# Kernel optimization log

Measured on AMD Instinct MI355X. Metric: run time of the kernel, lower is better.

## Reference

```python
import jax, jax.numpy as jnp
import numpy as np

NUM_INST = 3
N_NODES = 50000
IN_F = 128
HID = 64
HEADS = 4
HF = HEADS * HID  # 256
NEG_SLOPE = 0.2
BN_EPS = 1e-5


def setup_inputs() -> dict:
    key = jax.random.key(0)
    ks = jax.random.split(key, 10)
    sppmi = jax.random.normal(ks[0], (NUM_INST, N_NODES, IN_F), dtype=jnp.float32)
    edge_index = jax.random.randint(ks[1], (2, 800000), 0, N_NODES, dtype=jnp.int64)
    # Per-instance GATConv params (lin_src weight, att_src/att_dst, bias), BN, and Linear
    s = 1.0 / np.sqrt(IN_F)
    W = jax.random.uniform(ks[2], (NUM_INST, HF, IN_F), jnp.float32, -s, s)
    att_src = jax.random.uniform(ks[3], (NUM_INST, HEADS, HID), jnp.float32, -s, s)
    att_dst = jax.random.uniform(ks[4], (NUM_INST, HEADS, HID), jnp.float32, -s, s)
    bias = jnp.zeros((NUM_INST, HF), jnp.float32)
    bn_gamma = jnp.ones((NUM_INST, HF), jnp.float32)
    bn_beta = jnp.zeros((NUM_INST, HF), jnp.float32)
    bn_mean = jnp.zeros((NUM_INST, HF), jnp.float32)
    bn_var = jnp.ones((NUM_INST, HF), jnp.float32)
    s2 = 1.0 / np.sqrt(HF)
    lin_W = jax.random.uniform(ks[5], (NUM_INST, HID, HF), jnp.float32, -s2, s2)
    lin_b = jax.random.uniform(ks[6], (NUM_INST, HID), jnp.float32, -s2, s2)
    return {"sppmi": sppmi, "W": W, "att_src": att_src, "att_dst": att_dst,
            "bias": bias, "bn_gamma": bn_gamma, "bn_beta": bn_beta,
            "bn_mean": bn_mean, "bn_var": bn_var, "lin_W": lin_W,
            "lin_b": lin_b, "edge_index": edge_index}


def _gat_layer(x, W, a_src, a_dst, bias, gamma, beta, mean, var, linW, linb, src, dst):
    # GATConv (concat=True, add_self_loops already applied via src/dst)
    xw = (x @ W.T).reshape(N_NODES, HEADS, HID)            # [N,H,F]
    alpha_src = (xw * a_src).sum(-1)                        # [N,H]
    alpha_dst = (xw * a_dst).sum(-1)                        # [N,H]
    e = jax.nn.leaky_relu(alpha_src[src] + alpha_dst[dst], NEG_SLOPE)  # [E,H]
    m = jax.ops.segment_max(e, dst, num_segments=N_NODES)  # segment softmax over dst
    e = jnp.exp(e - m[dst])
    denom = jax.ops.segment_sum(e, dst, num_segments=N_NODES)
    alpha = e / (denom[dst] + 1e-16)                        # [E,H]
    msg = alpha[:, :, None] * xw[src]                       # [E,H,F] gather-attend
    out = jax.ops.segment_sum(msg, dst, num_segments=N_NODES)  # scatter-add
    out = out.reshape(N_NODES, HF) + bias
    # BatchNorm1d (eval: running stats), ReLU, Linear
    out = (out - mean) * jax.lax.rsqrt(var + BN_EPS) * gamma + beta
    out = jax.nn.relu(out)
    return out @ linW.T + linb                              # [N,HID]


def reference(sppmi, W, att_src, att_dst, bias, bn_gamma, bn_beta, bn_mean, bn_var, lin_W, lin_b, edge_index):
    loop = jnp.arange(N_NODES, dtype=edge_index.dtype)
    src = jnp.concatenate([edge_index[0], loop])
    dst = jnp.concatenate([edge_index[1], loop])
    all_emb = jnp.zeros((N_NODES, HID), jnp.float32)
    for i in range(NUM_INST):
        all_emb = all_emb + _gat_layer(sppmi[i], W[i], att_src[i], att_dst[i], bias[i],
                                       bn_gamma[i], bn_beta[i], bn_mean[i], bn_var[i],
                                       lin_W[i], lin_b[i], src, dst)
    out_1 = all_emb / jnp.linalg.norm(all_emb, axis=1, keepdims=True)
    return out_1
```

## Files before the change

kernel.cpp:

```cpp
#include <hip/hip_runtime.h>
#include <hip/hip_bf16.h>

#define N_NODES 50000
#define E0      800000
#define ET      850000
#define IN_F    128
#define HF      256
#define HID     64
#define NEG     0.2f
#define BN_EPSC 1e-5f
#define NSCAN_BLK 196

typedef __attribute__((ext_vector_type(8))) short bh8;
typedef __attribute__((ext_vector_type(4))) float fl4;
typedef __attribute__((ext_vector_type(8))) unsigned short us8;

__device__ __forceinline__ float lrelu(float x){ return x > 0.f ? x : NEG * x; }
__device__ __forceinline__ unsigned short f2b(float f){
  unsigned int x = __float_as_uint(f);
  unsigned int r = x + 0x7FFF + ((x >> 16) & 1);
  return (unsigned short)(r >> 16);
}
__device__ __forceinline__ float b2f(unsigned short u){
  return __uint_as_float((unsigned int)u << 16);
}

#define NW4 (3 * HF * IN_F / 4)
#define NL4 (3 * HID * HF / 4)
__global__ __launch_bounds__(256) void k_prep(const float* __restrict__ W, unsigned short* __restrict__ wb,
                                              const float* __restrict__ linW, unsigned short* __restrict__ lwb,
                                              const float* __restrict__ g, const float* __restrict__ b,
                                              const float* __restrict__ m, const float* __restrict__ v,
                                              float* __restrict__ scale, float* __restrict__ shiftv){
  int idx = blockIdx.x * 256 + threadIdx.x;
  if (idx < NW4){
    float4 x = ((const float4*)W)[idx];
    ((ushort4*)wb)[idx] = make_ushort4(f2b(x.x), f2b(x.y), f2b(x.z), f2b(x.w));
  } else if (idx < NW4 + NL4){
    int j = idx - NW4;
    float4 x = ((const float4*)linW)[j];
    ((ushort4*)lwb)[j] = make_ushort4(f2b(x.x), f2b(x.y), f2b(x.z), f2b(x.w));
  } else if (idx < NW4 + NL4 + 3 * HF){
    int i = idx - NW4 - NL4;
    float s = g[i] * rsqrtf(v[i] + BN_EPSC);
    scale[i] = s;
    shiftv[i] = b[i] - m[i] * s;
  }
}

__global__ void k_hist(const int* __restrict__ ei, int* __restrict__ counts){
  int e = blockIdx.x * 256 + threadIdx.x;
  if (e >= ET) return;
  int d = (e < E0) ? ei[E0 + e] : (e - E0);
  atomicAdd(&counts[d], 1);
}

__global__ __launch_bounds__(256) void k_bsum(const int* __restrict__ counts, int* __restrict__ bsums){
  int b = blockIdx.x;
  int t = threadIdx.x;
  int idx = b * 256 + t;
  int v = (idx < N_NODES) ? counts[idx] : 0;
  for (int m = 1; m < 64; m <<= 1) v += __shfl_xor(v, m, 64);
  __shared__ int ws[4];
  int lane = t & 63, w = t >> 6;
  if (lane == 0) ws[w] = v;
  __syncthreads();
  if (t == 0) bsums[b] = ws[0] + ws[1] + ws[2] + ws[3];
}

__global__ __launch_bounds__(256) void k_bscan(const int* __restrict__ bsums, int* __restrict__ bexcl,
                                               int* __restrict__ row_ptr){
  int t = threadIdx.x;
  int v = (t < NSCAN_BLK) ? bsums[t] : 0;
  int lane = t & 63, w = t >> 6;
  int incl = v;
  for (int m = 1; m < 64; m <<= 1){
    int n = __shfl_up(incl, m, 64);
    if (lane >= m) incl += n;
  }
  __shared__ int ws[4];
  if (lane == 63) ws[w] = incl;
  __syncthreads();
  if (t == 0){
    int r = 0;
    for (int j = 0; j < 4; ++j){ int x = ws[j]; ws[j] = r; r += x; }
  }
  __syncthreads();
  int excl = incl - v + ws[w];
  if (t < NSCAN_BLK) bexcl[t] = excl;
  if (t == 255) row_ptr[N_NODES] = excl + v;
}

__global__ __launch_bounds__(256) void k_sfinal(const int* __restrict__ counts,
                                                const int* __restrict__ bexcl,
                                                int* __restrict__ row_ptr, int* __restrict__ cursor){
  int b = blockIdx.x;
  int t = threadIdx.x;
  int idx = b * 256 + t;
  int v = (idx < N_NODES) ? counts[idx] : 0;
  int lane = t & 63, w = t >> 6;
  int incl = v;
  for (int m = 1; m < 64; m <<= 1){
    int n = __shfl_up(incl, m, 64);
    if (lane >= m) incl += n;
  }
  __shared__ int ws[4];
  if (lane == 63) ws[w] = incl;
  __syncthreads();
  if (t == 0){
    int r = 0;
    for (int j = 0; j < 4; ++j){ int x = ws[j]; ws[j] = r; r += x; }
  }
  __syncthreads();
  int excl = incl - v + ws[w];
  int pos = bexcl[b] + excl;
  if (idx < N_NODES){ row_ptr[idx] = pos; cursor[idx] = pos; }
}

__global__ void k_scatter(const int* __restrict__ ei, int* __restrict__ cursor,
                          int* __restrict__ csr_src){
  int e = blockIdx.x * 256 + threadIdx.x;
  if (e >= ET) return;
  int s, d;
  if (e < E0){ s = ei[e]; d = ei[E0 + e]; } else { s = e - E0; d = s; }
  int pos = atomicAdd(&cursor[d], 1);
  csr_src[pos] = s;
}

__global__ __launch_bounds__(256) void k_gemm1f(const float* __restrict__ sppmi,
                                                const unsigned short* __restrict__ wb,
                                                const float* __restrict__ att_src,
                                                const float* __restrict__ att_dst,
                                                unsigned short* __restrict__ xwb,
                                                float* __restrict__ as3, float* __restrict__ ad3){
  __shared__ unsigned char Asm[32 * 256];
  __shared__ unsigned char Bsm[256 * 256];
  int tid = threadIdx.x;
  int bx = blockIdx.x;
  int inst = bx / 1563;
  int m0 = (bx % 1563) * 32;
  const float* x = sppmi + (size_t)inst * N_NODES * IN_F;
  const unsigned short* wbv = wb + (size_t)inst * HF * IN_F;
  const float* asrc = att_src + inst * HF;
  const float* adst = att_dst + inst * HF;
  float* as_ = as3 + (size_t)inst * N_NODES * 4;
  float* ad_ = ad3 + (size_t)inst * N_NODES * 4;
  unsigned short* xw = xwb + (size_t)inst * N_NODES * HF;

  #pragma unroll
  for (int k = 0; k < 4; ++k){
    int c = k * 256 + tid;
    int row = c >> 5;
    int c4 = c & 31;
    int grow = m0 + row; if (grow >= N_NODES) grow = N_NODES - 1;
    float4 v = *(const float4*)&x[(size_t)grow * IN_F + c4 * 4];
    ushort4 o = make_ushort4(f2b(v.x), f2b(v.y), f2b(v.z), f2b(v.w));
    int colb = c4 * 8;
    int addr = row * 256 + ((colb & ~15) ^ ((row & 7) << 4)) + (colb & 15);
    *(ushort4*)(Asm + addr) = o;
  }
  #pragma unroll
  for (int k = 0; k < 16; ++k){
    int c = k * 256 + tid;
    int row = c >> 4;
    int colb = (c & 15) * 16;
    uint4 v = *(const uint4*)((const char*)wbv + (size_t)row * 256 + colb);
    *(uint4*)(Bsm + row * 256 + (colb ^ ((row & 7) << 4))) = v;
  }
  __syncthreads();

  int w = tid >> 6, lane = tid & 63;
  int l15 = lane & 15, l4 = lane >> 4;
  fl4 acc[2][4] = {};
  #pragma unroll
  for (int kk = 0; kk < 4; ++kk){
    bh8 af[2];
    #pragma unroll
    for (int m = 0; m < 2; ++m){
      int ar = m * 16 + l15;
      int ac = (kk * 64 + l4 * 16) ^ ((ar & 7) << 4);
      af[m] = *(const bh8*)(Asm + ar * 256 + ac);
    }
    bh8 bfv[4];
    #pragma unroll
    for (int n = 0; n < 4; ++n){
      int br = w * 64 + n * 16 + l15;
      int bc = (kk * 64 + l4 * 16) ^ ((br & 7) << 4);
      bfv[n] = *(const bh8*)(Bsm + br * 256 + bc);
    }
    #pragma unroll
    for (int m = 0; m < 2; ++m)
      #pragma unroll
      for (int n = 0; n < 4; ++n)
        acc[m][n] = __builtin_amdgcn_mfma_f32_16x16x32_bf16(af[m], bfv[n], acc[m][n], 0, 0, 0);
  }

  float asv[4], adv[4];
  #pragma unroll
  for (int n = 0; n < 4; ++n){
    int c = w * 64 + n * 16 + l15;
    asv[n] = asrc[c]; adv[n] = adst[c];
  }

  #pragma unroll
  for (int m = 0; m < 2; ++m){
    #pragma unroll
    for (int j = 0; j < 4; ++j){
      int grow = m0 + m * 16 + l4 * 4 + j;
      if (grow < N_NODES){
        #pragma unroll
        for (int n = 0; n < 4; ++n)
          xw[(size_t)grow * HF + w * 64 + n * 16 + l15] = f2b(acc[m][n][j]);
      }
      float ts = acc[m][0][j]*asv[0] + acc[m][1][j]*asv[1] + acc[m][2][j]*asv[2] + acc[m][3][j]*asv[3];
      float td = acc[m][0][j]*adv[0] + acc[m][1][j]*adv[1] + acc[m][2][j]*adv[2] + acc[m][3][j]*adv[3];
      #pragma unroll
      for (int mm = 1; mm < 16; mm <<= 1){ ts += __shfl_xor(ts, mm, 64); td += __shfl_xor(td, mm, 64); }
      if (l15 == 0 && grow < N_NODES){
        as_[grow * 4 + w] = ts;
        ad_[grow * 4 + w] = td;
      }
    }
  }
}

__global__ __launch_bounds__(256) void k_agg3(const unsigned short* __restrict__ xwb,
                     const float* __restrict__ as3, const float* __restrict__ ad3,
                     const int* __restrict__ row_ptr, const int* __restrict__ csr_src,
                     const float* __restrict__ bias, unsigned short* __restrict__ outb){
  __shared__ float eLds[4][4][65];
  __shared__ int   sLds[4][64];
  int bx = blockIdx.x;
  int inst = bx / 12500;
  int chunk = bx - inst * 12500;
  int w = threadIdx.x >> 6;
  int lane = threadIdx.x & 63;
  int node = chunk * 4 + w;
  int row0 = row_ptr[node];
  int deg = row_ptr[node + 1] - row0;
  const float* as_ = as3 + (size_t)inst * N_NODES * 4;
  const float* ad_ = ad3 + (size_t)inst * N_NODES * 4;
  float4 ad4 = *(const float4*)&ad_[node * 4];
  int h = lane >> 4;
  float accx = 0.f, accy = 0.f, accz = 0.f, accw = 0.f;
  float sh;
  const char* xwp = (const char*)(xwb + (size_t)inst * N_NODES * HF);
  int lb = lane * 8;

  if (deg <= 64){
    int soff = 0; float e0 = 0.f, e1 = 0.f, e2 = 0.f, e3 = 0.f;
    if (lane < deg){
      int sreg = csr_src[row0 + lane];
      soff = sreg * 512;
      float4 a4 = *(const float4*)&as_[sreg * 4];
      e0 = __expf(lrelu(a4.x + ad4.x));
      e1 = __expf(lrelu(a4.y + ad4.y));
      e2 = __expf(lrelu(a4.z + ad4.z));
      e3 = __expf(lrelu(a4.w + ad4.w));
    }
    sLds[w][lane] = soff;
    eLds[w][0][lane] = e0; eLds[w][1][lane] = e1;
    eLds[w][2][lane] = e2; eLds[w][3][lane] = e3;
    float s0 = e0, s1 = e1, s2 = e2, s3 = e3;
    for (int m = 1; m < 64; m <<= 1){
      s0 += __shfl_xor(s0, m, 64); s1 += __shfl_xor(s1, m, 64);
      s2 += __shfl_xor(s2, m, 64); s3 += __shfl_xor(s3, m, 64);
    }
    sh = (h == 0) ? s0 : (h == 1) ? s1 : (h == 2) ? s2 : s3;
    int q = 0;
    for (; q + 4 <= deg; q += 4){
      int o0 = sLds[w][q],   o1 = sLds[w][q+1];
      int o2 = sLds[w][q+2], o3 = sLds[w][q+3];
      float w0 = eLds[w][h][q],   w1 = eLds[w][h][q+1];
      float w2 = eLds[w][h][q+2], w3 = eLds[w][h][q+3];
      ushort4 u0 = *(const ushort4*)(xwp + o0 + lb);
      ushort4 u1 = *(const ushort4*)(xwp + o1 + lb);
      ushort4 u2 = *(const ushort4*)(xwp + o2 + lb);
      ushort4 u3 = *(const ushort4*)(xwp + o3 + lb);
      accx += w0*b2f(u0.x) + w1*b2f(u1.x) + w2*b2f(u2.x) + w3*b2f(u3.x);
      accy += w0*b2f(u0.y) + w1*b2f(u1.y) + w2*b2f(u2.y) + w3*b2f(u3.y);
      accz += w0*b2f(u0.z) + w1*b2f(u1.z) + w2*b2f(u2.z) + w3*b2f(u3.z);
      accw += w0*b2f(u0.w) + w1*b2f(u1.w) + w2*b2f(u2.w) + w3*b2f(u3.w);
    }
    for (; q < deg; ++q){
      int o0 = sLds[w][q];
      float wh = eLds[w][h][q];
      ushort4 u = *(const ushort4*)(xwp + o0 + lb);
      accx += wh * b2f(u.x); accy += wh * b2f(u.y);
      accz += wh * b2f(u.z); accw += wh * b2f(u.w);
    }
  } else {
    float s0 = 0.f, s1 = 0.f, s2 = 0.f, s3 = 0.f;
    for (int j = lane; j < deg; j += 64){
      int s = csr_src[row0 + j];
      float4 a4 = *(const float4*)&as_[s * 4];
      s0 += __expf(lrelu(a4.x + ad4.x));
      s1 += __expf(lrelu(a4.y + ad4.y));
      s2 += __expf(lrelu(a4.z + ad4.z));
      s3 += __expf(lrelu(a4.w + ad4.w));
    }
    for (int m = 1; m < 64; m <<= 1){
      s0 += __shfl_xor(s0, m, 64); s1 += __shfl_xor(s1, m, 64);
      s2 += __shfl_xor(s2, m, 64); s3 += __shfl_xor(s3, m, 64);
    }
    sh = (h == 0) ? s0 : (h == 1) ? s1 : (h == 2) ? s2 : s3;
    for (int jb = 0; jb < deg; jb += 64){
      int jj = jb + lane;
      int soff = 0; float e0 = 0.f, e1 = 0.f, e2 = 0.f, e3 = 0.f;
      if (jj < deg){
        int sreg = csr_src[row0 + jj];
        soff = sreg * 512;
        float4 a4 = *(const float4*)&as_[sreg * 4];
        e0 = __expf(lrelu(a4.x + ad4.x));
        e1 = __expf(lrelu(a4.y + ad4.y));
        e2 = __expf(lrelu(a4.z + ad4.z));
        e3 = __expf(lrelu(a4.w + ad4.w));
      }
      sLds[w][lane] = soff;
      eLds[w][0][lane] = e0; eLds[w][1][lane] = e1;
      eLds[w][2][lane] = e2; eLds[w][3][lane] = e3;
      __builtin_amdgcn_s_waitcnt(0);
      int lim = min(64, deg - jb);
      for (int q = 0; q < lim; ++q){
        int o0 = sLds[w][q];
        float wh = eLds[w][h][q];
        ushort4 u = *(const ushort4*)(xwp + o0 + lb);
        accx += wh * b2f(u.x); accy += wh * b2f(u.y);
        accz += wh * b2f(u.z); accw += wh * b2f(u.w);
      }
    }
  }
  float invh = 1.f / (sh + 1e-16f);
  const float* bi = bias + inst * HF;
  float4 b4 = *(const float4*)&bi[lane * 4];
  ushort4 o;
  o.x = f2b(accx * invh + b4.x); o.y = f2b(accy * invh + b4.y);
  o.z = f2b(accz * invh + b4.z); o.w = f2b(accw * invh + b4.w);
  *(ushort4*)&outb[(size_t)inst * N_NODES * HF + (size_t)node * HF + lane * 4] = o;
}

__global__ __launch_bounds__(256) void k_gemm2f(const unsigned short* __restrict__ obase,
                                                const unsigned short* __restrict__ lwb,
                                                const float* __restrict__ scale,
                                                const float* __restrict__ shiftv,
                                                const float* __restrict__ linb,
                                                float* __restrict__ outp){
  __shared__ unsigned char Asm[64 * 512];
  __shared__ unsigned char Bsm[64 * 512];
  int tid = threadIdx.x;
  int m0 = blockIdx.x * 64;
  int w = tid >> 6, lane = tid & 63;
  int l15 = lane & 15, l4 = lane >> 4;

  fl4 acc[4] = {};

  for (int i = 0; i < 3; ++i){
    if (i) __syncthreads();
    const unsigned short* A = obase + (size_t)i * N_NODES * HF;
    const float* sc = scale + i * HF;
    const float* sf = shiftv + i * HF;
    #pragma unroll
    for (int k = 0; k < 8; ++k){
      int c = k * 256 + tid;
      int row = c >> 5;
      int colb = (c & 31) * 16;
      int col = colb >> 1;
      int grow = m0 + row; if (grow >= N_NODES) grow = N_NODES - 1;
      us8 u = *(const us8*)&A[(size_t)grow * HF + col];
      float4 s0 = *(const float4*)&sc[col], s1 = *(const float4*)&sc[col + 4];
      float4 f0 = *(const float4*)&sf[col], f1 = *(const float4*)&sf[col + 4];
      us8 o;
      o[0] = f2b(fmaxf(0.f, b2f(u[0]) * s0.x + f0.x));
      o[1] = f2b(fmaxf(0.f, b2f(u[1]) * s0.y + f0.y));
      o[2] = f2b(fmaxf(0.f, b2f(u[2]) * s0.z + f0.z));
      o[3] = f2b(fmaxf(0.f, b2f(u[3]) * s0.w + f0.w));
      o[4] = f2b(fmaxf(0.f, b2f(u[4]) * s1.x + f1.x));
      o[5] = f2b(fmaxf(0.f, b2f(u[5]) * s1.y + f1.y));
      o[6] = f2b(fmaxf(0.f, b2f(u[6]) * s1.z + f1.z));
      o[7] = f2b(fmaxf(0.f, b2f(u[7]) * s1.w + f1.w));
      *(us8*)(Asm + row * 512 + (colb ^ ((row & 7) << 4))) = o;
    }
    const unsigned short* B = lwb + (size_t)i * HID * HF;
    #pragma unroll
    for (int k = 0; k < 8; ++k){
      int c = k * 256 + tid;
      int row = c >> 5;
      int colb = (c & 31) * 16;
      uint4 v = *(const uint4*)((const char*)B + (size_t)row * 512 + colb);
      *(uint4*)(Bsm + row * 512 + (colb ^ ((row & 7) << 4))) = v;
    }
    __syncthreads();
    #pragma unroll
    for (int kk = 0; kk < 8; ++kk){
      int ar = w * 16 + l15;
      int ac = (kk * 64 + l4 * 16) ^ ((ar & 7) << 4);
      bh8 af = *(const bh8*)(Asm + ar * 512 + ac);
      #pragma unroll
      for (int n = 0; n < 4; ++n){
        int br = n * 16 + l15;
        int bc = (kk * 64 + l4 * 16) ^ ((br & 7) << 4);
        bh8 bfv = *(const bh8*)(Bsm + br * 512 + bc);
        acc[n] = __builtin_amdgcn_mfma_f32_16x16x32_bf16(af, bfv, acc[n], 0, 0, 0);
      }
    }
  }
  float lbs[4];
  #pragma unroll
  for (int n = 0; n < 4; ++n){
    int c = n * 16 + l15;
    lbs[n] = linb[c] + linb[64 + c] + linb[128 + c];
  }
  #pragma unroll
  for (int j = 0; j < 4; ++j){
    float v0 = acc[0][j] + lbs[0];
    float v1 = acc[1][j] + lbs[1];
    float v2 = acc[2][j] + lbs[2];
    float v3 = acc[3][j] + lbs[3];
    float ss = v0*v0 + v1*v1 + v2*v2 + v3*v3;
    #pragma unroll
    for (int mm = 1; mm < 16; mm <<= 1) ss += __shfl_xor(ss, mm, 64);
    float rn = 1.f / sqrtf(ss);
    int grow = m0 + w * 16 + l4 * 4 + j;
    if (grow < N_NODES){
      float* op = outp + (size_t)grow * HID;
      op[l15]      = v0 * rn;
      op[16 + l15] = v1 * rn;
      op[32 + l15] = v2 * rn;
      op[48 + l15] = v3 * rn;
    }
  }
}

extern "C" void kernel_launch(void* const* d_in, const int* in_sizes, int n_in,
                              void* d_out, int out_size, void* d_ws, size_t ws_size,
                              hipStream_t stream){
  const float* sppmi   = (const float*)d_in[0];
  const float* W       = (const float*)d_in[1];
  const float* att_src = (const float*)d_in[2];
  const float* att_dst = (const float*)d_in[3];
  const float* bias    = (const float*)d_in[4];
  const float* bn_g    = (const float*)d_in[5];
  const float* bn_b    = (const float*)d_in[6];
  const float* bn_m    = (const float*)d_in[7];
  const float* bn_v    = (const float*)d_in[8];
  const float* lin_W   = (const float*)d_in[9];
  const float* lin_b   = (const float*)d_in[10];
  const int*   ei      = (const int*)d_in[11];

  char* ws = (char*)d_ws;
  size_t off = 0;
  auto alloc = [&](size_t bytes)->char*{ char* p = ws + off; off += (bytes + 255) & ~(size_t)255; return p; };
  unsigned short* wb   = (unsigned short*)alloc((size_t)3 * HF * IN_F * 2);
  unsigned short* lwb  = (unsigned short*)alloc((size_t)3 * HID * HF * 2);
  float* scale  = (float*)alloc((size_t)3 * HF * 4);
  float* shiftv = (float*)alloc((size_t)3 * HF * 4);
  unsigned short* xwb  = (unsigned short*)alloc((size_t)3 * N_NODES * HF * 2);
  unsigned short* outb = (unsigned short*)alloc((size_t)3 * N_NODES * HF * 2);
  float* as3    = (float*)alloc((size_t)3 * N_NODES * 4 * 4);
  float* ad3    = (float*)alloc((size_t)3 * N_NODES * 4 * 4);
  int* counts   = (int*)alloc((size_t)N_NODES * 4);
  int* row_ptr  = (int*)alloc((size_t)(N_NODES + 4) * 4);
  int* cursor   = (int*)alloc((size_t)N_NODES * 4);
  int* csr      = (int*)alloc((size_t)ET * 4);
  int* bsums    = (int*)alloc((size_t)NSCAN_BLK * 4);
  int* bexcl    = (int*)alloc((size_t)NSCAN_BLK * 4);

  hipMemsetAsync(counts, 0, (size_t)N_NODES * 4, stream);

  k_prep<<<147, 256, 0, stream>>>(W, wb, lin_W, lwb, bn_g, bn_b, bn_m, bn_v, scale, shiftv);

  k_hist<<<(ET + 255) / 256, 256, 0, stream>>>(ei, counts);
  k_bsum<<<NSCAN_BLK, 256, 0, stream>>>(counts, bsums);
  k_bscan<<<1, 256, 0, stream>>>(bsums, bexcl, row_ptr);
  k_sfinal<<<NSCAN_BLK, 256, 0, stream>>>(counts, bexcl, row_ptr, cursor);
  k_scatter<<<(ET + 255) / 256, 256, 0, stream>>>(ei, cursor, csr);

  k_gemm1f<<<3 * 1563, 256, 0, stream>>>(sppmi, wb, att_src, att_dst, xwb, as3, ad3);
  k_agg3<<<37500, 256, 0, stream>>>(xwb, as3, ad3, row_ptr, csr, bias, outb);
  k_gemm2f<<<782, 256, 0, stream>>>(outb, lwb, scale, shiftv, lin_b, (float*)d_out);
}
```

Measured before the change: 361.2 us.

## Permute xw column layout for vector stores, fuse scan kernels, persistent aggregation grid

The first GEMM now writes its bf16 output as packed ushort4 stores in a permuted column order instead of four scattered 2-byte stores. The bias, BN scale/shift and linear weights are pre-permuted in the prep kernel to match that order. The single-block block-scan kernel is merged into the final scan kernel, with every block redundantly scanning the block sums, which removes one launch. The aggregation kernel becomes a grid-stride persistent loop over 2048 blocks instead of 37500, trading launch and scheduling overhead for possible load imbalance.

Measured after the change: 371.1 us. +2.7%, slower.

```diff
diff --git a/kernel.cpp b/kernel.cpp
--- a/kernel.cpp
+++ b/kernel.cpp
@@ -10,6 +10,7 @@
 #define NEG     0.2f
 #define BN_EPSC 1e-5f
 #define NSCAN_BLK 196
+#define NCHUNKS 37500
 
 typedef __attribute__((ext_vector_type(8))) short bh8;
 typedef __attribute__((ext_vector_type(4))) float fl4;
@@ -23,6 +24,11 @@
 }
 __device__ __forceinline__ float b2f(unsigned short u){
   return __uint_as_float((unsigned int)u << 16);
+}
+
+__device__ __forceinline__ int perm_true(int cp){
+  int blk = cp & ~63, r = cp & 63;
+  return blk + (r & 3) * 16 + (r >> 2);
 }
 
 #define NW4 (3 * HF * IN_F / 4)
@@ -31,20 +37,33 @@
                                               const float* __restrict__ linW, unsigned short* __restrict__ lwb,
                                               const float* __restrict__ g, const float* __restrict__ b,
                                               const float* __restrict__ m, const float* __restrict__ v,
-                                              float* __restrict__ scale, float* __restrict__ shiftv){
+                                              const float* __restrict__ bias,
+                                              float* __restrict__ scale, float* __restrict__ shiftv,
+                                              float* __restrict__ bias_p){
   int idx = blockIdx.x * 256 + threadIdx.x;
   if (idx < NW4){
     float4 x = ((const float4*)W)[idx];
     ((ushort4*)wb)[idx] = make_ushort4(f2b(x.x), f2b(x.y), f2b(x.z), f2b(x.w));
   } else if (idx < NW4 + NL4){
     int j = idx - NW4;
-    float4 x = ((const float4*)linW)[j];
-    ((ushort4*)lwb)[j] = make_ushort4(f2b(x.x), f2b(x.y), f2b(x.z), f2b(x.w));
+    int j4 = j * 4;
+    int irow = j4 >> 8;
+    int cp = j4 & 255;
+    int blk = cp & ~63, l15 = (cp & 63) >> 2;
+    const float* src = linW + (size_t)irow * HF + blk + l15;
+    ushort4 o = make_ushort4(f2b(src[0]), f2b(src[16]), f2b(src[32]), f2b(src[48]));
+    ((ushort4*)lwb)[j] = o;
   } else if (idx < NW4 + NL4 + 3 * HF){
     int i = idx - NW4 - NL4;
-    float s = g[i] * rsqrtf(v[i] + BN_EPSC);
+    int inst = i >> 8, cp = i & 255;
+    int c = inst * HF + perm_true(cp);
+    float s = g[c] * rsqrtf(v[c] + BN_EPSC);
     scale[i] = s;
-    shiftv[i] = b[i] - m[i] * s;
+    shiftv[i] = b[c] - m[c] * s;
+  } else if (idx < NW4 + NL4 + 6 * HF){
+    int i = idx - NW4 - NL4 - 3 * HF;
+    int inst = i >> 8, cp = i & 255;
+    bias_p[i] = bias[inst * HF + perm_true(cp)];
   }
 }
 
@@ -68,52 +87,37 @@
   if (t == 0) bsums[b] = ws[0] + ws[1] + ws[2] + ws[3];
 }
 
-__global__ __launch_bounds__(256) void k_bscan(const int* __restrict__ bsums, int* __restrict__ bexcl,
-                                               int* __restrict__ row_ptr){
-  int t = threadIdx.x;
-  int v = (t < NSCAN_BLK) ? bsums[t] : 0;
+__global__ __launch_bounds__(256) void k_sfinal(const int* __restrict__ counts,
+                                                const int* __restrict__ bsums,
+                                                int* __restrict__ row_ptr, int* __restrict__ cursor){
+  __shared__ int bex[256];
+  __shared__ int ws0[4];
+  __shared__ int ws[4];
+  int b = blockIdx.x, t = threadIdx.x;
   int lane = t & 63, w = t >> 6;
+  {
+    int v = (t < NSCAN_BLK) ? bsums[t] : 0;
+    int incl = v;
+    for (int m = 1; m < 64; m <<= 1){ int n = __shfl_up(incl, m, 64); if (lane >= m) incl += n; }
+    if (lane == 63) ws0[w] = incl;
+    __syncthreads();
+    if (t == 0){ int r = 0; for (int j = 0; j < 4; ++j){ int x = ws0[j]; ws0[j] = r; r += x; } }
+    __syncthreads();
+    int excl = incl - v + ws0[w];
+    bex[t] = excl;
+    if (b == 0 && t == 255) row_ptr[N_NODES] = excl + v;
+    __syncthreads();
+  }
+  int idx = b * 256 + t;
+  int v = (idx < N_NODES) ? counts[idx] : 0;
   int incl = v;
-  for (int m = 1; m < 64; m <<= 1){
-    int n = __shfl_up(incl, m, 64);
-    if (lane >= m) incl += n;
-  }
-  __shared__ int ws[4];
+  for (int m = 1; m < 64; m <<= 1){ int n = __shfl_up(incl, m, 64); if (lane >= m) incl += n; }
   if (lane == 63) ws[w] = incl;
   __syncthreads();
-  if (t == 0){
-    int r = 0;
-    for (int j = 0; j < 4; ++j){ int x = ws[j]; ws[j] = r; r += x; }
-  }
+  if (t == 0){ int r = 0; for (int j = 0; j < 4; ++j){ int x = ws[j]; ws[j] = r; r += x; } }
   __syncthreads();
   int excl = incl - v + ws[w];
-  if (t < NSCAN_BLK) bexcl[t] = excl;
-  if (t == 255) row_ptr[N_NODES] = excl + v;
-}
-
-__global__ __launch_bounds__(256) void k_sfinal(const int* __restrict__ counts,
-                                                const int* __restrict__ bexcl,
-                                                int* __restrict__ row_ptr, int* __restrict__ cursor){
-  int b = blockIdx.x;
-  int t = threadIdx.x;
-  int idx = b * 256 + t;
-  int v = (idx < N_NODES) ? counts[idx] : 0;
-  int lane = t & 63, w = t >> 6;
-  int incl = v;
-  for (int m = 1; m < 64; m <<= 1){
-    int n = __shfl_up(incl, m, 64);
-    if (lane >= m) incl += n;
-  }
-  __shared__ int ws[4];
-  if (lane == 63) ws[w] = incl;
-  __syncthreads();
-  if (t == 0){
-    int r = 0;
-    for (int j = 0; j < 4; ++j){ int x = ws[j]; ws[j] = r; r += x; }
-  }
-  __syncthreads();
-  int excl = incl - v + ws[w];
-  int pos = bexcl[b] + excl;
+  int pos = bex[b] + excl;
   if (idx < N_NODES){ row_ptr[idx] = pos; cursor[idx] = pos; }
 }
 
@@ -208,9 +212,9 @@
     for (int j = 0; j < 4; ++j){
       int grow = m0 + m * 16 + l4 * 4 + j;
       if (grow < N_NODES){
-        #pragma unroll
-        for (int n = 0; n < 4; ++n)
-          xw[(size_t)grow * HF + w * 64 + n * 16 + l15] = f2b(acc[m][n][j]);
+        ushort4 o4 = make_ushort4(f2b(acc[m][0][j]), f2b(acc[m][1][j]),
+                                  f2b(acc[m][2][j]), f2b(acc[m][3][j]));
+        *(ushort4*)(xw + (size_t)grow * HF + w * 64 + l15 * 4) = o4;
       }
       float ts = acc[m][0][j]*asv[0] + acc[m][1][j]*asv[1] + acc[m][2][j]*asv[2] + acc[m][3][j]*asv[3];
       float td = acc[m][0][j]*adv[0] + acc[m][1][j]*adv[1] + acc[m][2][j]*adv[2] + acc[m][3][j]*adv[3];
@@ -227,89 +231,32 @@
 __global__ __launch_bounds__(256) void k_agg3(const unsigned short* __restrict__ xwb,
                      const float* __restrict__ as3, const float* __restrict__ ad3,
                      const int* __restrict__ row_ptr, const int* __restrict__ csr_src,
-                     const float* __restrict__ bias, unsigned short* __restrict__ outb){
+                     const float* __restrict__ bias_p, unsigned short* __restrict__ outb){
   __shared__ float eLds[4][4][65];
   __shared__ int   sLds[4][64];
-  int bx = blockIdx.x;
-  int inst = bx / 12500;
-  int chunk = bx - inst * 12500;
   int w = threadIdx.x >> 6;
   int lane = threadIdx.x & 63;
-  int node = chunk * 4 + w;
-  int row0 = row_ptr[node];
-  int deg = row_ptr[node + 1] - row0;
-  const float* as_ = as3 + (size_t)inst * N_NODES * 4;
-  const float* ad_ = ad3 + (size_t)inst * N_NODES * 4;
-  float4 ad4 = *(const float4*)&ad_[node * 4];
   int h = lane >> 4;
-  float accx = 0.f, accy = 0.f, accz = 0.f, accw = 0.f;
-  float sh;
-  const char* xwp = (const char*)(xwb + (size_t)inst * N_NODES * HF);
   int lb = lane * 8;
 
-  if (deg <= 64){
-    int soff = 0; float e0 = 0.f, e1 = 0.f, e2 = 0.f, e3 = 0.f;
-    if (lane < deg){
-      int sreg = csr_src[row0 + lane];
-      soff = sreg * 512;
-      float4 a4 = *(const float4*)&as_[sreg * 4];
-      e0 = __expf(lrelu(a4.x + ad4.x));
-      e1 = __expf(lrelu(a4.y + ad4.y));
-      e2 = __expf(lrelu(a4.z + ad4.z));
-      e3 = __expf(lrelu(a4.w + ad4.w));
-    }
-    sLds[w][lane] = soff;
-    eLds[w][0][lane] = e0; eLds[w][1][lane] = e1;
-    eLds[w][2][lane] = e2; eLds[w][3][lane] = e3;
-    float s0 = e0, s1 = e1, s2 = e2, s3 = e3;
-    for (int m = 1; m < 64; m <<= 1){
-      s0 += __shfl_xor(s0, m, 64); s1 += __shfl_xor(s1, m, 64);
-      s2 += __shfl_xor(s2, m, 64); s3 += __shfl_xor(s3, m, 64);
-    }
-    sh = (h == 0) ? s0 : (h == 1) ? s1 : (h == 2) ? s2 : s3;
-    int q = 0;
-    for (; q + 4 <= deg; q += 4){
-      int o0 = sLds[w][q],   o1 = sLds[w][q+1];
-      int o2 = sLds[w][q+2], o3 = sLds[w][q+3];
-      float w0 = eLds[w][h][q],   w1 = eLds[w][h][q+1];
-      float w2 = eLds[w][h][q+2], w3 = eLds[w][h][q+3];
-      ushort4 u0 = *(const ushort4*)(xwp + o0 + lb);
-      ushort4 u1 = *(const ushort4*)(xwp + o1 + lb);
-      ushort4 u2 = *(const ushort4*)(xwp + o2 + lb);
-      ushort4 u3 = *(const ushort4*)(xwp + o3 + lb);
-      accx += w0*b2f(u0.x) + w1*b2f(u1.x) + w2*b2f(u2.x) + w3*b2f(u3.x);
-      accy += w0*b2f(u0.y) + w1*b2f(u1.y) + w2*b2f(u2.y) + w3*b2f(u3.y);
-      accz += w0*b2f(u0.z) + w1*b2f(u1.z) + w2*b2f(u2.z) + w3*b2f(u3.z);
-      accw += w0*b2f(u0.w) + w1*b2f(u1.w) + w2*b2f(u2.w) + w3*b2f(u3.w);
-    }
-    for (; q < deg; ++q){
-      int o0 = sLds[w][q];
-      float wh = eLds[w][h][q];
-      ushort4 u = *(const ushort4*)(xwp + o0 + lb);
-      accx += wh * b2f(u.x); accy += wh * b2f(u.y);
-      accz += wh * b2f(u.z); accw += wh * b2f(u.w);
-    }
-  } else {
-    float s0 = 0.f, s1 = 0.f, s2 = 0.f, s3 = 0.f;
-    for (int j = lane; j < deg; j += 64){
-      int s = csr_src[row0 + j];
-      float4 a4 = *(const float4*)&as_[s * 4];
-      s0 += __expf(lrelu(a4.x + ad4.x));
-      s1 += __expf(lrelu(a4.y + ad4.y));
-      s2 += __expf(lrelu(a4.z + ad4.z));
-      s3 += __expf(lrelu(a4.w + ad4.w));
-    }
-    for (int m = 1; m < 64; m <<= 1){
-      s0 += __shfl_xor(s0, m, 64); s1 += __shfl_xor(s1, m, 64);
-      s2 += __shfl_xor(s2, m, 64); s3 += __shfl_xor(s3, m, 64);
-    }
-    sh = (h == 0) ? s0 : (h == 1) ? s1 : (h == 2) ? s2 : s3;
-    for (int jb = 0; jb < deg; jb += 64){
-      int jj = jb + lane;
+  for (int c = blockIdx.x; c < NCHUNKS; c += gridDim.x){
+    int inst = c / 12500;
+    int chunk = c - inst * 12500;
+    int node = chunk * 4 + w;
+    int row0 = row_ptr[node];
+    int deg = row_ptr[node + 1] - row0;
+    const float* as_ = as3 + (size_t)inst * N_NODES * 4;
+    const float* ad_ = ad3 + (size_t)inst * N_NODES * 4;
+    float4 ad4 = *(const float4*)&ad_[node * 4];
+    float accx = 0.f, accy = 0.f, accz = 0.f, accw = 0.f;
+    float sh;
+    const char* xwp = (const char*)(xwb + (size_t)inst * N_NODES * HF);
+
+    if (deg <= 64){
       int soff = 0; float e0 = 0.f, e1 = 0.f, e2 = 0.f, e3 = 0.f;
-      if (jj < deg){
-        int sreg = csr_src[row0 + jj];
-        soff = sreg * 512;
+      if (lane < deg){
+        int sreg = csr_src[row0 + lane];
+        soff = sreg << 9;
         float4 a4 = *(const float4*)&as_[sreg * 4];
         e0 = __expf(lrelu(a4.x + ad4.x));
         e1 = __expf(lrelu(a4.y + ad4.y));
@@ -319,24 +266,83 @@
       sLds[w][lane] = soff;
       eLds[w][0][lane] = e0; eLds[w][1][lane] = e1;
       eLds[w][2][lane] = e2; eLds[w][3][lane] = e3;
-      __builtin_amdgcn_s_waitcnt(0);
-      int lim = min(64, deg - jb);
-      for (int q = 0; q < lim; ++q){
+      float s0 = e0, s1 = e1, s2 = e2, s3 = e3;
+      for (int m = 1; m < 64; m <<= 1){
+        s0 += __shfl_xor(s0, m, 64); s1 += __shfl_xor(s1, m, 64);
+        s2 += __shfl_xor(s2, m, 64); s3 += __shfl_xor(s3, m, 64);
+      }
+      sh = (h == 0) ? s0 : (h == 1) ? s1 : (h == 2) ? s2 : s3;
+      int q = 0;
+      for (; q + 4 <= deg; q += 4){
+        int o0 = sLds[w][q],   o1 = sLds[w][q+1];
+        int o2 = sLds[w][q+2], o3 = sLds[w][q+3];
+        float w0 = eLds[w][h][q],   w1 = eLds[w][h][q+1];
+        float w2 = eLds[w][h][q+2], w3 = eLds[w][h][q+3];
+        ushort4 u0 = *(const ushort4*)(xwp + o0 + lb);
+        ushort4 u1 = *(const ushort4*)(xwp + o1 + lb);
+        ushort4 u2 = *(const ushort4*)(xwp + o2 + lb);
+        ushort4 u3 = *(const ushort4*)(xwp + o3 + lb);
+        accx += w0*b2f(u0.x) + w1*b2f(u1.x) + w2*b2f(u2.x) + w3*b2f(u3.x);
+        accy += w0*b2f(u0.y) + w1*b2f(u1.y) + w2*b2f(u2.y) + w3*b2f(u3.y);
+        accz += w0*b2f(u0.z) + w1*b2f(u1.z) + w2*b2f(u2.z) + w3*b2f(u3.z);
+        accw += w0*b2f(u0.w) + w1*b2f(u1.w) + w2*b2f(u2.w) + w3*b2f(u3.w);
+      }
+      for (; q < deg; ++q){
         int o0 = sLds[w][q];
         float wh = eLds[w][h][q];
         ushort4 u = *(const ushort4*)(xwp + o0 + lb);
         accx += wh * b2f(u.x); accy += wh * b2f(u.y);
         accz += wh * b2f(u.z); accw += wh * b2f(u.w);
       }
-    }
-  }
-  float invh = 1.f / (sh + 1e-16f);
-  const float* bi = bias + inst * HF;
-  float4 b4 = *(const float4*)&bi[lane * 4];
-  ushort4 o;
-  o.x = f2b(accx * invh + b4.x); o.y = f2b(accy * invh + b4.y);
-  o.z = f2b(accz * invh + b4.z); o.w = f2b(accw * invh + b4.w);
-  *(ushort4*)&outb[(size_t)inst * N_NODES * HF + (size_t)node * HF + lane * 4] = o;
+    } else {
+      float s0 = 0.f, s1 = 0.f, s2 = 0.f, s3 = 0.f;
+      for (int j = lane; j < deg; j += 64){
+        int s = csr_src[row0 + j];
+        float4 a4 = *(const float4*)&as_[s * 4];
+        s0 += __expf(lrelu(a4.x + ad4.x));
+        s1 += __expf(lrelu(a4.y + ad4.y));
+        s2 += __expf(lrelu(a4.z + ad4.z));
+        s3 += __expf(lrelu(a4.w + ad4.w));
+      }
+      for (int m = 1; m < 64; m <<= 1){
+        s0 += __shfl_xor(s0, m, 64); s1 += __shfl_xor(s1, m, 64);
+        s2 += __shfl_xor(s2, m, 64); s3 += __shfl_xor(s3, m, 64);
+      }
+      sh = (h == 0) ? s0 : (h == 1) ? s1 : (h == 2) ? s2 : s3;
+      for (int jb = 0; jb < deg; jb += 64){
+        int jj = jb + lane;
+        int soff = 0; float e0 = 0.f, e1 = 0.f, e2 = 0.f, e3 = 0.f;
+        if (jj < deg){
+          int sreg = csr_src[row0 + jj];
+          soff = sreg << 9;
+          float4 a4 = *(const float4*)&as_[sreg * 4];
+          e0 = __expf(lrelu(a4.x + ad4.x));
+          e1 = __expf(lrelu(a4.y + ad4.y));
+          e2 = __expf(lrelu(a4.z + ad4.z));
+          e3 = __expf(lrelu(a4.w + ad4.w));
+        }
+        sLds[w][lane] = soff;
+        eLds[w][0][lane] = e0; eLds[w][1][lane] = e1;
+        eLds[w][2][lane] = e2; eLds[w][3][lane] = e3;
+        __builtin_amdgcn_s_waitcnt(0);
+        int lim = min(64, deg - jb);
+        for (int q = 0; q < lim; ++q){
+          int o0 = sLds[w][q];
+          float wh = eLds[w][h][q];
+          ushort4 u = *(const ushort4*)(xwp + o0 + lb);
+          accx += wh * b2f(u.x); accy += wh * b2f(u.y);
+          accz += wh * b2f(u.z); accw += wh * b2f(u.w);
+        }
+      }
+    }
+    float invh = 1.f / (sh + 1e-16f);
+    const float* bi = bias_p + inst * HF;
+    float4 b4 = *(const float4*)&bi[lane * 4];
+    ushort4 o;
+    o.x = f2b(accx * invh + b4.x); o.y = f2b(accy * invh + b4.y);
+    o.z = f2b(accz * invh + b4.z); o.w = f2b(accw * invh + b4.w);
+    *(ushort4*)&outb[(size_t)inst * N_NODES * HF + (size_t)node * HF + lane * 4] = o;
+  }
 }
 
 __global__ __launch_bounds__(256) void k_gemm2f(const unsigned short* __restrict__ obase,
@@ -454,6 +460,7 @@
   unsigned short* lwb  = (unsigned short*)alloc((size_t)3 * HID * HF * 2);
   float* scale  = (float*)alloc((size_t)3 * HF * 4);
   float* shiftv = (float*)alloc((size_t)3 * HF * 4);
+  float* bias_p = (float*)alloc((size_t)3 * HF * 4);
   unsigned short* xwb  = (unsigned short*)alloc((size_t)3 * N_NODES * HF * 2);
   unsigned short* outb = (unsigned short*)alloc((size_t)3 * N_NODES * HF * 2);
   float* as3    = (float*)alloc((size_t)3 * N_NODES * 4 * 4);
@@ -463,19 +470,18 @@
   int* cursor   = (int*)alloc((size_t)N_NODES * 4);
   int* csr      = (int*)alloc((size_t)ET * 4);
   int* bsums    = (int*)alloc((size_t)NSCAN_BLK * 4);
-  int* bexcl    = (int*)alloc((size_t)NSCAN_BLK * 4);
 
   hipMemsetAsync(counts, 0, (size_t)N_NODES * 4, stream);
 
-  k_prep<<<147, 256, 0, stream>>>(W, wb, lin_W, lwb, bn_g, bn_b, bn_m, bn_v, scale, shiftv);
+  k_prep<<<150, 256, 0, stream>>>(W, wb, lin_W, lwb, bn_g, bn_b, bn_m, bn_v, bias,
+                                  scale, shiftv, bias_p);
 
   k_hist<<<(ET + 255) / 256, 256, 0, stream>>>(ei, counts);
   k_bsum<<<NSCAN_BLK, 256, 0, stream>>>(counts, bsums);
-  k_bscan<<<1, 256, 0, stream>>>(bsums, bexcl, row_ptr);
-  k_sfinal<<<NSCAN_BLK, 256, 0, stream>>>(counts, bexcl, row_ptr, cursor);
+  k_sfinal<<<NSCAN_BLK, 256, 0, stream>>>(counts, bsums, row_ptr, cursor);
   k_scatter<<<(ET + 255) / 256, 256, 0, stream>>>(ei, cursor, csr);
 
   k_gemm1f<<<3 * 1563, 256, 0, stream>>>(sppmi, wb, att_src, att_dst, xwb, as3, ad3);
-  k_agg3<<<37500, 256, 0, stream>>>(xwb, as3, ad3, row_ptr, csr, bias, outb);
+  k_agg3<<<2048, 256, 0, stream>>>(xwb, as3, ad3, row_ptr, csr, bias_p, outb);
   k_gemm2f<<<782, 256, 0, stream>>>(outb, lwb, scale, shiftv, lin_b, (float*)d_out);
 }
```
